# Kernel optimization log

Measured on AMD Instinct MI355X. Metric: run time of the kernel, lower is better.

The kernel has to match this reference:

```python
import jax, jax.numpy as jnp
import numpy as np

B, S, D = 8, 1024, 1024
H = 16
D_HEAD = D // H
RANK = 256
NC = 64
NE = 64
KC = 16  # top_k_compress
KE = 8   # top_k_expand


def setup_inputs() -> dict:
    key = jax.random.key(0)
    ks = jax.random.split(key, 9)
    rn = lambda k, sh, s=1.0: jax.random.normal(k, sh, jnp.float32) * s
    return {
        "x": rn(ks[0], (B, S, D)),
        "importance": jax.random.uniform(ks[1], (B, S), jnp.float32),
        "W_compress": rn(ks[2], (NC, D), 1.0 / np.sqrt(D)),
        "W_Q": rn(ks[3], (NE, D), 1.0 / np.sqrt(D)),
        "W_K": rn(ks[4], (NE, D), 1.0 / np.sqrt(D)),
        "W_V": rn(ks[5], (NE, D), 1.0 / np.sqrt(D)),
        "compress_neurons": rn(ks[6], (NC, D, RANK), 1.0 / np.sqrt(D)),
        "expand_pool": rn(ks[7], (NE, RANK, D), 1.0 / np.sqrt(RANK)),
        "W_O": rn(ks[8], (D, D), 1.0 / np.sqrt(D)),
    }


def _route(x, importance, W, k):
    """Per-token softmax router, importance-aggregated, top-k renormalized."""
    pref = jax.nn.softmax(jnp.einsum('bsd,nd->bsn', x, W), axis=-1)  # [B,S,n]
    w = jnp.einsum('bs,bsn->bn', importance, pref)                   # [B,n]
    w = w / (w.sum(-1, keepdims=True) + 1e-8)
    tw, ti = jax.lax.top_k(w, k)                                     # [B,k]
    tw = tw / (tw.sum(-1, keepdims=True) + 1e-8)
    return tw, ti


def reference(x, importance, W_compress, W_Q, W_K, W_V, compress_neurons, expand_pool, W_O):
    # --- GlobalRouters.get_attention_weights ---
    cw, ci = _route(x, importance, W_compress, KC)
    qw, qi = _route(x, importance, W_Q, KE)
    kw, ki = _route(x, importance, W_K, KE)
    vw, vi = _route(x, importance, W_V, KE)

    # --- NeuronCircuit.forward ---
    # gather + mix compress neurons: [B,KC,D,R] -> [B,D,R]
    shared_c = jnp.einsum('bk,bkdr->bdr', cw, compress_neurons[ci])
    h = jnp.einsum('bsd,bdr->bsr', x, shared_c)  # [B,S,R]

    eQ = jnp.einsum('bk,bkrd->brd', qw, expand_pool[qi])
    eK = jnp.einsum('bk,bkrd->brd', kw, expand_pool[ki])
    eV = jnp.einsum('bk,bkrd->brd', vw, expand_pool[vi])

    def heads(t):  # [B,S,D] -> [B,H,S,d_head]
        return t.reshape(B, S, H, D_HEAD).transpose(0, 2, 1, 3)

    Q = heads(jnp.einsum('bsr,brd->bsd', h, eQ))
    K = heads(jnp.einsum('bsr,brd->bsd', h, eK))
    V = heads(jnp.einsum('bsr,brd->bsd', h, eV))

    scale = 1.0 / np.sqrt(D_HEAD)
    scores = jnp.einsum('bhqd,bhkd->bhqk', Q, K) * scale
    causal = jnp.tril(jnp.ones((S, S), dtype=bool))
    scores = jnp.where(causal, scores, jnp.finfo(scores.dtype).min)
    attn = jax.nn.softmax(scores, axis=-1)
    out = jnp.einsum('bhqk,bhkd->bhqd', attn, V)
    out = out.transpose(0, 2, 1, 3).reshape(B, S, D)
    return jnp.einsum('bsd,ed->bse', out, W_O)  # expand_O (Linear, no bias)
```

## Files before the change

kernel.cpp:

```cpp
#include <hip/hip_runtime.h>

typedef __attribute__((ext_vector_type(8))) short short8;
typedef __attribute__((ext_vector_type(4))) short short4v;
typedef __attribute__((ext_vector_type(4))) float f32x4;
typedef unsigned short u16;
typedef unsigned int u32;

__device__ __forceinline__ float bf2f(u16 h) {
    return __uint_as_float(((u32)h) << 16);
}
__device__ __forceinline__ u16 f2bf(float f) {
    u32 u = __float_as_uint(f);
    u32 r = u + 0x7fffu + ((u >> 16) & 1u);
    return (u16)(r >> 16);
}
__device__ __forceinline__ u32 pack_bf(float a, float b) {
    return __builtin_amdgcn_perm(__float_as_uint(b), __float_as_uint(a), 0x07060302u);
}

__device__ __forceinline__ void async_copy16(const void* g, void* l) {
    __builtin_amdgcn_global_load_lds(
        (const __attribute__((address_space(1))) void*)g,
        (__attribute__((address_space(3))) void*)l, 16, 0, 0);
}

__global__ __launch_bounds__(256) void cvt_split(
    const float* __restrict__ in, u16* __restrict__ hi, u16* __restrict__ lo, int n4)
{
    int i = blockIdx.x * 256 + threadIdx.x;
    if (i >= n4) return;
    float4 v = ((const float4*)in)[i];
    short4v h, l;
    float vv[4] = {v.x, v.y, v.z, v.w};
#pragma unroll
    for (int j = 0; j < 4; j++) {
        u16 hb = f2bf(vv[j]);
        h[j] = (short)hb;
        l[j] = (short)f2bf(vv[j] - bf2f(hb));
    }
    ((short4v*)hi)[i] = h;
    ((short4v*)lo)[i] = l;
}

__global__ __launch_bounds__(256) void cvt_split_w4(
    const float* __restrict__ w0, const float* __restrict__ w1,
    const float* __restrict__ w2, const float* __restrict__ w3,
    u16* __restrict__ hi, u16* __restrict__ lo)
{
    const int r = blockIdx.x >> 6;
    const float* src = (r == 0) ? w0 : (r == 1) ? w1 : (r == 2) ? w2 : w3;
    int i = (blockIdx.x & 63) * 256 + threadIdx.x;
    float4 v = ((const float4*)src)[i];
    short4v h, l;
    float vv[4] = {v.x, v.y, v.z, v.w};
#pragma unroll
    for (int j = 0; j < 4; j++) {
        u16 hb = f2bf(vv[j]);
        h[j] = (short)hb;
        l[j] = (short)f2bf(vv[j] - bf2f(hb));
    }
    ((short4v*)(hi + (long)r * 65536))[i] = h;
    ((short4v*)(lo + (long)r * 65536))[i] = l;
}

__global__ __launch_bounds__(256) void cvt_bf(
    const float* __restrict__ in, u16* __restrict__ out, int n4)
{
    int i = blockIdx.x * 256 + threadIdx.x;
    if (i >= n4) return;
    float4 v = ((const float4*)in)[i];
    short4v h;
    h[0] = (short)f2bf(v.x); h[1] = (short)f2bf(v.y);
    h[2] = (short)f2bf(v.z); h[3] = (short)f2bf(v.w);
    ((short4v*)out)[i] = h;
}

template <typename CT>
__global__ __launch_bounds__(256) void gemm_bt(
    const u16* __restrict__ A, long lda, long bsA,
    const u16* __restrict__ Bm, long ldb, long bsB,
    CT* __restrict__ C, long ldc, long bsC, int K, float cscale)
{
    __shared__ __align__(16) u16 lsA[128 * 32];
    __shared__ __align__(16) u16 lsB[128 * 32];
    const int tid = threadIdx.x;
    const int wave = tid >> 6, lane = tid & 63;
    const int quad = lane >> 4, l15 = lane & 15;
    const int wm = wave >> 1, wn = wave & 1;
    const long m0 = (long)blockIdx.x * 128, n0 = (long)blockIdx.y * 128;
    A  += (long)blockIdx.z * bsA;
    Bm += (long)blockIdx.z * bsB;
    C  += (long)blockIdx.z * bsC;
    const int srow = lane >> 2, scol = (lane & 3) * 8;

    f32x4 acc[4][4];
#pragma unroll
    for (int i = 0; i < 4; i++)
#pragma unroll
        for (int j = 0; j < 4; j++) acc[i][j] = (f32x4){0.f, 0.f, 0.f, 0.f};

    const u16* ga0 = A + (m0 + (wave * 2 + 0) * 16 + srow) * lda + scol;
    const u16* ga1 = A + (m0 + (wave * 2 + 1) * 16 + srow) * lda + scol;
    const u16* gb0 = Bm + (n0 + (wave * 2 + 0) * 16 + srow) * ldb + scol;
    const u16* gb1 = Bm + (n0 + (wave * 2 + 1) * 16 + srow) * ldb + scol;
    u16* la0 = &lsA[(wave * 2 + 0) * 512];
    u16* la1 = &lsA[(wave * 2 + 1) * 512];
    u16* lb0 = &lsB[(wave * 2 + 0) * 512];
    u16* lb1 = &lsB[(wave * 2 + 1) * 512];

    for (int kk = 0; kk < K; kk += 32) {
        async_copy16(ga0 + kk, la0);
        async_copy16(ga1 + kk, la1);
        async_copy16(gb0 + kk, lb0);
        async_copy16(gb1 + kk, lb1);
        __syncthreads();
        short8 af[4], bf[4];
#pragma unroll
        for (int mt = 0; mt < 4; mt++)
            af[mt] = *(const short8*)&lsA[(wm * 64 + mt * 16 + l15) * 32 + quad * 8];
#pragma unroll
        for (int nt = 0; nt < 4; nt++)
            bf[nt] = *(const short8*)&lsB[(wn * 64 + nt * 16 + l15) * 32 + quad * 8];
#pragma unroll
        for (int mt = 0; mt < 4; mt++)
#pragma unroll
            for (int nt = 0; nt < 4; nt++)
                acc[mt][nt] = __builtin_amdgcn_mfma_f32_16x16x32_bf16(
                    af[mt], bf[nt], acc[mt][nt], 0, 0, 0);
        __syncthreads();
    }
#pragma unroll
    for (int mt = 0; mt < 4; mt++) {
        const long rowb = m0 + wm * 64 + mt * 16 + quad * 4;
#pragma unroll
        for (int nt = 0; nt < 4; nt++) {
            const long col = n0 + wn * 64 + nt * 16 + l15;
#pragma unroll
            for (int r = 0; r < 4; r++) {
                const float v = acc[mt][nt][r] * cscale;
                if constexpr (sizeof(CT) == 2)
                    C[(rowb + r) * ldc + col] = f2bf(v);
                else
                    C[(rowb + r) * ldc + col] = v;
            }
        }
    }
}

__global__ __launch_bounds__(256) void gemm_router(
    const u16* __restrict__ Ah, const u16* __restrict__ Al,
    const u16* __restrict__ Bh, const u16* __restrict__ Bl,
    float* __restrict__ C)
{
    __shared__ __align__(16) u16 lsA[128 * 32];
    __shared__ __align__(16) u16 lsB[128 * 32];
    const int tid = threadIdx.x;
    const int wave = tid >> 6, lane = tid & 63;
    const int quad = lane >> 4, l15 = lane & 15;
    const int wm = wave >> 1, wn = wave & 1;
    const long m0 = (long)blockIdx.x * 128, n0 = (long)blockIdx.y * 128;
    const int srow = lane >> 2, scol = (lane & 3) * 8;
    const long offA = (m0 + (wave * 2) * 16 + srow) * 1024 + scol;
    const long offB = (n0 + (wave * 2) * 16 + srow) * 1024 + scol;
    u16* la0 = &lsA[(wave * 2 + 0) * 512];
    u16* la1 = &lsA[(wave * 2 + 1) * 512];
    u16* lb0 = &lsB[(wave * 2 + 0) * 512];
    u16* lb1 = &lsB[(wave * 2 + 1) * 512];

    f32x4 acc[4][4];
#pragma unroll
    for (int i = 0; i < 4; i++)
#pragma unroll
        for (int j = 0; j < 4; j++) acc[i][j] = (f32x4){0.f, 0.f, 0.f, 0.f};

    for (int seg = 0; seg < 3; seg++) {
        const u16* A = (seg == 1) ? Al : Ah;
        const u16* B = (seg == 2) ? Bl : Bh;
        const u16* ga = A + offA;
        const u16* gb = B + offB;
        for (int kk = 0; kk < 1024; kk += 32) {
            async_copy16(ga + kk, la0);
            async_copy16(ga + 16384 + kk, la1);
            async_copy16(gb + kk, lb0);
            async_copy16(gb + 16384 + kk, lb1);
            __syncthreads();
            short8 af[4], bf[4];
#pragma unroll
            for (int mt = 0; mt < 4; mt++)
                af[mt] = *(const short8*)&lsA[(wm * 64 + mt * 16 + l15) * 32 + quad * 8];
#pragma unroll
            for (int nt = 0; nt < 4; nt++)
                bf[nt] = *(const short8*)&lsB[(wn * 64 + nt * 16 + l15) * 32 + quad * 8];
#pragma unroll
            for (int mt = 0; mt < 4; mt++)
#pragma unroll
                for (int nt = 0; nt < 4; nt++)
                    acc[mt][nt] = __builtin_amdgcn_mfma_f32_16x16x32_bf16(
                        af[mt], bf[nt], acc[mt][nt], 0, 0, 0);
            __syncthreads();
        }
    }
#pragma unroll
    for (int mt = 0; mt < 4; mt++) {
        const long rowb = m0 + wm * 64 + mt * 16 + quad * 4;
#pragma unroll
        for (int nt = 0; nt < 4; nt++) {
            const long col = n0 + wn * 64 + nt * 16 + l15;
#pragma unroll
            for (int r = 0; r < 4; r++)
                C[(rowb + r) * 256 + col] = acc[mt][nt][r];
        }
    }
}

__global__ __launch_bounds__(128) void router_agg(
    const float* __restrict__ logits, const float* __restrict__ imp,
    float* __restrict__ w_raw)
{
    __shared__ float pref[32][257];
    const int tid = threadIdx.x;
    const int tl = tid >> 2, r = tid & 3;
    const int s = blockIdx.x * 32 + tl;
    const int b = s >> 10;
    const float* lp = logits + (long)s * 256 + r * 64;
    float v[64];
#pragma unroll
    for (int i = 0; i < 16; i++) {
        float4 f = ((const float4*)lp)[i];
        v[i * 4 + 0] = f.x; v[i * 4 + 1] = f.y;
        v[i * 4 + 2] = f.z; v[i * 4 + 3] = f.w;
    }
    float mx = v[0];
#pragma unroll
    for (int i = 1; i < 64; i++) mx = fmaxf(mx, v[i]);
    float sum = 0.f;
#pragma unroll
    for (int i = 0; i < 64; i++) { v[i] = __expf(v[i] - mx); sum += v[i]; }
    const float scale = imp[s] / sum;
#pragma unroll
    for (int i = 0; i < 64; i++) pref[tl][r * 64 + i] = v[i] * scale;
    __syncthreads();
#pragma unroll
    for (int half = 0; half < 2; half++) {
        const int idx = tid + half * 128;
        const int r2 = idx >> 6, n = idx & 63;
        float acc = 0.f;
#pragma unroll 8
        for (int t = 0; t < 32; t++) acc += pref[t][r2 * 64 + n];
        atomicAdd(&w_raw[(r2 * 8 + b) * 64 + n], acc);
    }
}

__global__ void topk_kernel(const float* __restrict__ w_raw,
                            float* __restrict__ topw, int* __restrict__ topi)
{
    const int r = blockIdx.x >> 3, b = blockIdx.x & 7;
    const int lane = threadIdx.x;
    const int k = (r == 0) ? 16 : 8;
    float w = w_raw[(r * 8 + b) * 64 + lane];
    float tot = w;
    for (int o2 = 32; o2 >= 1; o2 >>= 1) tot += __shfl_xor(tot, o2);
    w = w / (tot + 1e-8f);
    __shared__ float tw[16];
    __shared__ int ti[16];
    float cur = w;
    float ssum = 0.f;
    for (int j = 0; j < k; j++) {
        float m = cur; int mi = lane;
        for (int o2 = 32; o2 >= 1; o2 >>= 1) {
            float om = __shfl_xor(m, o2); int oi = __shfl_xor(mi, o2);
            if (om > m || (om == m && oi < mi)) { m = om; mi = oi; }
        }
        if (lane == 0) { tw[j] = m; ti[j] = mi; }
        ssum += m;
        if (lane == mi) cur = -1e30f;
    }
    __syncthreads();
    if (lane < 16) {
        topw[(r * 8 + b) * 16 + lane] = (lane < k) ? tw[lane] / (ssum + 1e-8f) : 0.f;
        topi[(r * 8 + b) * 16 + lane] = (lane < k) ? ti[lane] : 0;
    }
}

__global__ __launch_bounds__(256) void gather_mix(
    const float* __restrict__ pool, const float* __restrict__ topw,
    const int* __restrict__ topi, u16* __restrict__ out,
    int I, int J, int k)
{
    __shared__ float tile[64][65];
    const int b = blockIdx.z;
    const long IJ = (long)I * J;
    const int i0 = blockIdx.x * 64, j0 = blockIdx.y * 64;
    const float* tw = topw + b * 16;
    const int* ti = topi + b * 16;
    const int tid = threadIdx.x;
    const int il = tid >> 2, jg = tid & 3;
    float acc[16];
#pragma unroll
    for (int m = 0; m < 16; m++) acc[m] = 0.f;
    for (int kk = 0; kk < k; kk++) {
        const float wgt = tw[kk];
        const long n = ti[kk];
        const float* src = pool + n * IJ + (long)(i0 + il) * J + j0 + jg * 16;
        float4 a0 = ((const float4*)src)[0];
        float4 a1 = ((const float4*)src)[1];
        float4 a2 = ((const float4*)src)[2];
        float4 a3 = ((const float4*)src)[3];
        acc[0] += wgt * a0.x;  acc[1] += wgt * a0.y;
        acc[2] += wgt * a0.z;  acc[3] += wgt * a0.w;
        acc[4] += wgt * a1.x;  acc[5] += wgt * a1.y;
        acc[6] += wgt * a1.z;  acc[7] += wgt * a1.w;
        acc[8] += wgt * a2.x;  acc[9] += wgt * a2.y;
        acc[10] += wgt * a2.z; acc[11] += wgt * a2.w;
        acc[12] += wgt * a3.x; acc[13] += wgt * a3.y;
        acc[14] += wgt * a3.z; acc[15] += wgt * a3.w;
    }
#pragma unroll
    for (int m = 0; m < 16; m++) tile[il][jg * 16 + m] = acc[m];
    __syncthreads();
    const int jl = tid >> 2, ig = tid & 3;
    short8 o0, o1;
#pragma unroll
    for (int m = 0; m < 8; m++) {
        o0[m] = (short)f2bf(tile[ig * 16 + m][jl]);
        o1[m] = (short)f2bf(tile[ig * 16 + 8 + m][jl]);
    }
    u16* dst = out + (long)b * IJ + (long)(j0 + jl) * I + i0 + ig * 16;
    *(short8*)dst = o0;
    *(short8*)(dst + 8) = o1;
}

__global__ __launch_bounds__(256, 2) void flash_attn(
    const u16* __restrict__ Qg, const u16* __restrict__ Kg,
    const u16* __restrict__ Vt, u16* __restrict__ Og)
{
    __shared__ __align__(16) u16 plds[4][32 * 72];
    const int tid = threadIdx.x;
    const int wv = tid >> 6, lane = tid & 63;
    const int quad = lane >> 4, l15 = lane & 15;
    const int bidx = blockIdx.x;
    const int bh = bidx & 127;
    const int qt = ((bidx >> 7) << 2) + wv;
    const int hh = bh & 15, bb = bh >> 4;
    const long SD = 1024L * 1024L;
    const u16* Qb = Qg + (long)bb * SD + hh * 64;
    const u16* Kb = Kg + (long)bb * SD + hh * 64;
    const u16* Vb = Vt + (long)bb * SD + (long)hh * 64 * 1024;
    u16* myp = plds[wv];

    const int q0 = qt * 32;

    short8 qf[2][2];
#pragma unroll
    for (int mt = 0; mt < 2; mt++)
#pragma unroll
        for (int kb = 0; kb < 2; kb++)
            qf[mt][kb] = *(const short8*)(Qb + (long)(q0 + mt * 16 + l15) * 1024 + kb * 32 + quad * 8);

    f32x4 o[2][4];
    float mrow[2] = {-3e38f, -3e38f}, lrow[2] = {0.f, 0.f};
#pragma unroll
    for (int mt = 0; mt < 2; mt++)
#pragma unroll
        for (int nt = 0; nt < 4; nt++) o[mt][nt] = (f32x4){0.f, 0.f, 0.f, 0.f};

    const int ntile = (q0 + 95) >> 6;
    short8 kf[4][2], kn[4][2];
#pragma unroll
    for (int kt = 0; kt < 4; kt++)
#pragma unroll
        for (int kb = 0; kb < 2; kb++)
            kf[kt][kb] = *(const short8*)(Kb + (long)(kt * 16 + l15) * 1024 + kb * 32 + quad * 8);

    for (int it = 0; it < ntile; it++) {
        const int k2 = it * 64;
        const bool last = (it == ntile - 1);
        f32x4 st[4][2];
#pragma unroll
        for (int kt = 0; kt < 4; kt++)
#pragma unroll
            for (int q_ = 0; q_ < 2; q_++) {
                f32x4 z = (f32x4){0.f, 0.f, 0.f, 0.f};
                z = __builtin_amdgcn_mfma_f32_16x16x32_bf16(kf[kt][0], qf[q_][0], z, 0, 0, 0);
                z = __builtin_amdgcn_mfma_f32_16x16x32_bf16(kf[kt][1], qf[q_][1], z, 0, 0, 0);
                st[kt][q_] = z;
            }
        short8 vf[4][2];
#pragma unroll
        for (int nt = 0; nt < 4; nt++)
#pragma unroll
            for (int kh = 0; kh < 2; kh++)
                vf[nt][kh] = *(const short8*)(Vb + (long)(nt * 16 + l15) * 1024 + k2 + kh * 32 + quad * 8);
        if (it + 1 < ntile) {
#pragma unroll
            for (int kt = 0; kt < 4; kt++)
#pragma unroll
                for (int kb = 0; kb < 2; kb++)
                    kn[kt][kb] = *(const short8*)(Kb + (long)(k2 + 64 + kt * 16 + l15) * 1024 + kb * 32 + quad * 8);
        }
        float am[2];
#pragma unroll
        for (int q_ = 0; q_ < 2; q_++) {
            if (last) {
#pragma unroll
                for (int kt = 0; kt < 4; kt++)
#pragma unroll
                    for (int r = 0; r < 4; r++)
                        if (k2 + kt * 16 + quad * 4 + r > q0 + q_ * 16 + l15)
                            st[kt][q_][r] = -3e38f;
            }
            float cm = -3e38f;
#pragma unroll
            for (int kt = 0; kt < 4; kt++)
#pragma unroll
                for (int r = 0; r < 4; r++) cm = fmaxf(cm, st[kt][q_][r]);
            cm = fmaxf(cm, __shfl_xor(cm, 16));
            cm = fmaxf(cm, __shfl_xor(cm, 32));
            const float mn = fmaxf(mrow[q_], cm);
            am[q_] = exp2f(mrow[q_] - mn);
            mrow[q_] = mn;
            const float moff = 0.00281502f - mn;
            float rs = 0.f;
#pragma unroll
            for (int kt = 0; kt < 4; kt++) {
                float p0 = exp2f(st[kt][q_][0] + moff);
                float p1 = exp2f(st[kt][q_][1] + moff);
                float p2 = exp2f(st[kt][q_][2] + moff);
                float p3 = exp2f(st[kt][q_][3] + moff);
                rs += (p0 + p1) + (p2 + p3);
                u32 w0 = pack_bf(p0, p1);
                u32 w1 = pack_bf(p2, p3);
                *(uint2*)&myp[(q_ * 16 + l15) * 72 + kt * 16 + quad * 4] = make_uint2(w0, w1);
            }
            rs += __shfl_xor(rs, 16);
            rs += __shfl_xor(rs, 32);
            lrow[q_] = lrow[q_] * am[q_] + rs;
        }
        float av[2][4];
#pragma unroll
        for (int mt = 0; mt < 2; mt++)
#pragma unroll
            for (int r = 0; r < 4; r++)
                av[mt][r] = __shfl(am[mt], quad * 4 + r);
        asm volatile("s_waitcnt lgkmcnt(0)" ::: "memory");
        short8 pf0[2], pf1[2];
#pragma unroll
        for (int kh = 0; kh < 2; kh++) {
            pf0[kh] = *(const short8*)&myp[(l15) * 72 + kh * 32 + quad * 8];
            pf1[kh] = *(const short8*)&myp[(16 + l15) * 72 + kh * 32 + quad * 8];
        }
#pragma unroll
        for (int mt = 0; mt < 2; mt++)
#pragma unroll
            for (int nt = 0; nt < 4; nt++)
#pragma unroll
                for (int r = 0; r < 4; r++) o[mt][nt][r] *= av[mt][r];
#pragma unroll
        for (int nt = 0; nt < 4; nt++)
#pragma unroll
            for (int kh = 0; kh < 2; kh++) {
                o[0][nt] = __builtin_amdgcn_mfma_f32_16x16x32_bf16(pf0[kh], vf[nt][kh], o[0][nt], 0, 0, 0);
                o[1][nt] = __builtin_amdgcn_mfma_f32_16x16x32_bf16(pf1[kh], vf[nt][kh], o[1][nt], 0, 0, 0);
            }
        if (it + 1 < ntile) {
#pragma unroll
            for (int kt = 0; kt < 4; kt++)
#pragma unroll
                for (int kb = 0; kb < 2; kb++) kf[kt][kb] = kn[kt][kb];
        }
    }
#pragma unroll
    for (int mt = 0; mt < 2; mt++)
#pragma unroll
        for (int r = 0; r < 4; r++) {
            const float li = 1.0f / __shfl(lrow[mt], quad * 4 + r);
            const long row = q0 + mt * 16 + quad * 4 + r;
#pragma unroll
            for (int nt = 0; nt < 4; nt++)
                Og[(long)bb * SD + row * 1024 + hh * 64 + nt * 16 + l15] =
                    f2bf(o[mt][nt][r] * li);
        }
}

extern "C" void kernel_launch(void* const* d_in, const int* in_sizes, int n_in,
                              void* d_out, int out_size, void* d_ws, size_t ws_size,
                              hipStream_t stream)
{
    const float* x   = (const float*)d_in[0];
    const float* imp = (const float*)d_in[1];
    const float* cn  = (const float*)d_in[6];
    const float* ep  = (const float*)d_in[7];
    const float* Wo  = (const float*)d_in[8];
    float* outp = (float*)d_out;
    char* ws = (char*)d_ws;

    u16* xh = (u16*)d_out;
    u16* xl = xh + 8388608;

    u16*   Wh     = (u16*)(ws + 0);
    u16*   Wl     = (u16*)(ws + 524288);
    u16*   Wobf   = (u16*)(ws + 1048576);
    float* w_raw  = (float*)(ws + 3145728);
    float* topw   = (float*)(ws + 3153920);
    int*   topi   = (int*)(ws + 3155968);
    float* logits = (float*)(ws + 4194304);
    u16*   scT    = (u16*)(ws + 12582912);
    u16*   eQT    = (u16*)(ws + 16777216);
    u16*   Kb     = (u16*)(ws + 4194304);
    u16*   hbuf   = (u16*)(ws + 20971520);
    u16*   eKT    = (u16*)(ws + 25165824);
    u16*   eVT    = (u16*)(ws + 29360128);
    u16*   Qb     = (u16*)(ws + 33554432);
    u16*   VTb    = (u16*)(ws + 50331648);
    u16*   aout   = (u16*)(ws + 67108864);

    cvt_split<<<dim3(8192), 256, 0, stream>>>(x, xh, xl, 2097152);
    cvt_split_w4<<<dim3(256), 256, 0, stream>>>(
        (const float*)d_in[2], (const float*)d_in[3],
        (const float*)d_in[4], (const float*)d_in[5], Wh, Wl);
    cvt_bf<<<dim3(1024), 256, 0, stream>>>(Wo, Wobf, 262144);
    hipMemsetAsync(w_raw, 0, 4 * 8 * 64 * 4, stream);

    gemm_router<<<dim3(64, 2, 1), 256, 0, stream>>>(xh, xl, Wh, Wl, logits);
    router_agg<<<dim3(256), 128, 0, stream>>>(logits, imp, w_raw);
    topk_kernel<<<dim3(32), 64, 0, stream>>>(w_raw, topw, topi);
    gather_mix<<<dim3(16, 4, 8), 256, 0, stream>>>(cn, topw + 0 * 128, topi + 0 * 128, scT, 1024, 256, 16);
    gather_mix<<<dim3(4, 16, 8), 256, 0, stream>>>(ep, topw + 1 * 128, topi + 1 * 128, eQT, 256, 1024, 8);
    gather_mix<<<dim3(4, 16, 8), 256, 0, stream>>>(ep, topw + 2 * 128, topi + 2 * 128, eKT, 256, 1024, 8);
    gather_mix<<<dim3(4, 16, 8), 256, 0, stream>>>(ep, topw + 3 * 128, topi + 3 * 128, eVT, 256, 1024, 8);
    gemm_bt<u16><<<dim3(8, 2, 8), 256, 0, stream>>>(
        xh, 1024, 1048576, scT, 1024, 262144, hbuf, 256, 262144, 1024, 1.0f);
    gemm_bt<u16><<<dim3(8, 8, 8), 256, 0, stream>>>(
        hbuf, 256, 262144, eQT, 256, 262144, Qb, 1024, 1048576, 256, 0.180336880111f);
    gemm_bt<u16><<<dim3(8, 8, 8), 256, 0, stream>>>(
        hbuf, 256, 262144, eKT, 256, 262144, Kb, 1024, 1048576, 256, 1.0f);
    gemm_bt<u16><<<dim3(8, 8, 8), 256, 0, stream>>>(
        eVT, 256, 262144, hbuf, 256, 262144, VTb, 1024, 1048576, 256, 1.0f);
    flash_attn<<<dim3(1024), 256, 0, stream>>>(Qb, Kb, VTb, aout);
    gemm_bt<float><<<dim3(64, 8, 1), 256, 0, stream>>>(
        aout, 1024, 0, Wobf, 1024, 0, outp, 1024, 0, 1024, 1.0f);
}
```

Measured before the change: 454.3 us.

## Merge QKV gather-mix and GEMM launches, reorder and retune flash attention

The three expand-pool gather_mix launches become one gather_mix3 launch with a 24-deep z grid, and the three Q/K/V projection GEMMs become one gemm_qkv launch that selects operands by blockIdx.z. This cuts launch overhead and gives each launch a bigger grid to fill the GPU. Flash attention now schedules the longest causal query tiles first, drops the register double-buffered K prefetch in favour of in-loop loads, and raises its occupancy hint from 2 to 3 blocks per CU. Losing the prefetch may expose K load latency, which the extra occupancy is meant to hide.

```diff
diff --git a/kernel.cpp b/kernel.cpp
--- a/kernel.cpp
+++ b/kernel.cpp
@@ -143,6 +143,77 @@
                 else
                     C[(rowb + r) * ldc + col] = v;
             }
+        }
+    }
+}
+
+__global__ __launch_bounds__(256) void gemm_qkv(
+    const u16* __restrict__ hbuf, const u16* __restrict__ eQT,
+    const u16* __restrict__ eKT, const u16* __restrict__ eVT,
+    u16* __restrict__ Qb, u16* __restrict__ Kb, u16* __restrict__ VTb)
+{
+    __shared__ __align__(16) u16 lsA[128 * 32];
+    __shared__ __align__(16) u16 lsB[128 * 32];
+    const int z = blockIdx.z;
+    const int sel = z >> 3, bbz = z & 7;
+    const long ab = (long)bbz * 262144;
+    const u16* A  = ((sel == 2) ? eVT : hbuf) + ab;
+    const u16* Bm = ((sel == 0) ? eQT : (sel == 1) ? eKT : hbuf) + ab;
+    u16* C = ((sel == 0) ? Qb : (sel == 1) ? Kb : VTb) + (long)bbz * 1048576;
+    const float cscale = (sel == 0) ? 0.180336880111f : 1.0f;
+
+    const int tid = threadIdx.x;
+    const int wave = tid >> 6, lane = tid & 63;
+    const int quad = lane >> 4, l15 = lane & 15;
+    const int wm = wave >> 1, wn = wave & 1;
+    const long m0 = (long)blockIdx.x * 128, n0 = (long)blockIdx.y * 128;
+    const int srow = lane >> 2, scol = (lane & 3) * 8;
+
+    f32x4 acc[4][4];
+#pragma unroll
+    for (int i = 0; i < 4; i++)
+#pragma unroll
+        for (int j = 0; j < 4; j++) acc[i][j] = (f32x4){0.f, 0.f, 0.f, 0.f};
+
+    const u16* ga0 = A + (m0 + (wave * 2 + 0) * 16 + srow) * 256 + scol;
+    const u16* ga1 = A + (m0 + (wave * 2 + 1) * 16 + srow) * 256 + scol;
+    const u16* gb0 = Bm + (n0 + (wave * 2 + 0) * 16 + srow) * 256 + scol;
+    const u16* gb1 = Bm + (n0 + (wave * 2 + 1) * 16 + srow) * 256 + scol;
+    u16* la0 = &lsA[(wave * 2 + 0) * 512];
+    u16* la1 = &lsA[(wave * 2 + 1) * 512];
+    u16* lb0 = &lsB[(wave * 2 + 0) * 512];
+    u16* lb1 = &lsB[(wave * 2 + 1) * 512];
+
+    for (int kk = 0; kk < 256; kk += 32) {
+        async_copy16(ga0 + kk, la0);
+        async_copy16(ga1 + kk, la1);
+        async_copy16(gb0 + kk, lb0);
+        async_copy16(gb1 + kk, lb1);
+        __syncthreads();
+        short8 af[4], bf[4];
+#pragma unroll
+        for (int mt = 0; mt < 4; mt++)
+            af[mt] = *(const short8*)&lsA[(wm * 64 + mt * 16 + l15) * 32 + quad * 8];
+#pragma unroll
+        for (int nt = 0; nt < 4; nt++)
+            bf[nt] = *(const short8*)&lsB[(wn * 64 + nt * 16 + l15) * 32 + quad * 8];
+#pragma unroll
+        for (int mt = 0; mt < 4; mt++)
+#pragma unroll
+            for (int nt = 0; nt < 4; nt++)
+                acc[mt][nt] = __builtin_amdgcn_mfma_f32_16x16x32_bf16(
+                    af[mt], bf[nt], acc[mt][nt], 0, 0, 0);
+        __syncthreads();
+    }
+#pragma unroll
+    for (int mt = 0; mt < 4; mt++) {
+        const long rowb = m0 + wm * 64 + mt * 16 + quad * 4;
+#pragma unroll
+        for (int nt = 0; nt < 4; nt++) {
+            const long col = n0 + wn * 64 + nt * 16 + l15;
+#pragma unroll
+            for (int r = 0; r < 4; r++)
+                C[(rowb + r) * 1024 + col] = f2bf(acc[mt][nt][r] * cscale);
         }
     }
 }
@@ -330,7 +401,57 @@
     *(short8*)(dst + 8) = o1;
 }
 
-__global__ __launch_bounds__(256, 2) void flash_attn(
+__global__ __launch_bounds__(256) void gather_mix3(
+    const float* __restrict__ pool, const float* __restrict__ topw,
+    const int* __restrict__ topi, u16* __restrict__ eQT,
+    u16* __restrict__ eKT, u16* __restrict__ eVT)
+{
+    __shared__ float tile[64][65];
+    const int z = blockIdx.z;
+    const int r = z >> 3, b = z & 7;
+    u16* out = (r == 0) ? eQT : (r == 1) ? eKT : eVT;
+    const long IJ = 262144;
+    const int i0 = blockIdx.x * 64, j0 = blockIdx.y * 64;
+    const float* tw = topw + (1 + r) * 128 + b * 16;
+    const int* ti = topi + (1 + r) * 128 + b * 16;
+    const int tid = threadIdx.x;
+    const int il = tid >> 2, jg = tid & 3;
+    float acc[16];
+#pragma unroll
+    for (int m = 0; m < 16; m++) acc[m] = 0.f;
+    for (int kk = 0; kk < 8; kk++) {
+        const float wgt = tw[kk];
+        const long n = ti[kk];
+        const float* src = pool + n * IJ + (long)(i0 + il) * 1024 + j0 + jg * 16;
+        float4 a0 = ((const float4*)src)[0];
+        float4 a1 = ((const float4*)src)[1];
+        float4 a2 = ((const float4*)src)[2];
+        float4 a3 = ((const float4*)src)[3];
+        acc[0] += wgt * a0.x;  acc[1] += wgt * a0.y;
+        acc[2] += wgt * a0.z;  acc[3] += wgt * a0.w;
+        acc[4] += wgt * a1.x;  acc[5] += wgt * a1.y;
+        acc[6] += wgt * a1.z;  acc[7] += wgt * a1.w;
+        acc[8] += wgt * a2.x;  acc[9] += wgt * a2.y;
+        acc[10] += wgt * a2.z; acc[11] += wgt * a2.w;
+        acc[12] += wgt * a3.x; acc[13] += wgt * a3.y;
+        acc[14] += wgt * a3.z; acc[15] += wgt * a3.w;
+    }
+#pragma unroll
+    for (int m = 0; m < 16; m++) tile[il][jg * 16 + m] = acc[m];
+    __syncthreads();
+    const int jl = tid >> 2, ig = tid & 3;
+    short8 o0, o1;
+#pragma unroll
+    for (int m = 0; m < 8; m++) {
+        o0[m] = (short)f2bf(tile[ig * 16 + m][jl]);
+        o1[m] = (short)f2bf(tile[ig * 16 + 8 + m][jl]);
+    }
+    u16* dst = out + (long)b * IJ + (long)(j0 + jl) * 256 + i0 + ig * 16;
+    *(short8*)dst = o0;
+    *(short8*)(dst + 8) = o1;
+}
+
+__global__ __launch_bounds__(256, 3) void flash_attn(
     const u16* __restrict__ Qg, const u16* __restrict__ Kg,
     const u16* __restrict__ Vt, u16* __restrict__ Og)
 {
@@ -340,7 +461,7 @@
     const int quad = lane >> 4, l15 = lane & 15;
     const int bidx = blockIdx.x;
     const int bh = bidx & 127;
-    const int qt = ((bidx >> 7) << 2) + wv;
+    const int qt = ((7 - (bidx >> 7)) << 2) + wv;
     const int hh = bh & 15, bb = bh >> 4;
     const long SD = 1024L * 1024L;
     const u16* Qb = Qg + (long)bb * SD + hh * 64;
@@ -365,16 +486,16 @@
         for (int nt = 0; nt < 4; nt++) o[mt][nt] = (f32x4){0.f, 0.f, 0.f, 0.f};
 
     const int ntile = (q0 + 95) >> 6;
-    short8 kf[4][2], kn[4][2];
-#pragma unroll
-    for (int kt = 0; kt < 4; kt++)
-#pragma unroll
-        for (int kb = 0; kb < 2; kb++)
-            kf[kt][kb] = *(const short8*)(Kb + (long)(kt * 16 + l15) * 1024 + kb * 32 + quad * 8);
 
     for (int it = 0; it < ntile; it++) {
         const int k2 = it * 64;
         const bool last = (it == ntile - 1);
+        short8 kf[4][2];
+#pragma unroll
+        for (int kt = 0; kt < 4; kt++)
+#pragma unroll
+            for (int kb = 0; kb < 2; kb++)
+                kf[kt][kb] = *(const short8*)(Kb + (long)(k2 + kt * 16 + l15) * 1024 + kb * 32 + quad * 8);
         f32x4 st[4][2];
 #pragma unroll
         for (int kt = 0; kt < 4; kt++)
@@ -391,13 +512,6 @@
 #pragma unroll
             for (int kh = 0; kh < 2; kh++)
                 vf[nt][kh] = *(const short8*)(Vb + (long)(nt * 16 + l15) * 1024 + k2 + kh * 32 + quad * 8);
-        if (it + 1 < ntile) {
-#pragma unroll
-            for (int kt = 0; kt < 4; kt++)
-#pragma unroll
-                for (int kb = 0; kb < 2; kb++)
-                    kn[kt][kb] = *(const short8*)(Kb + (long)(k2 + 64 + kt * 16 + l15) * 1024 + kb * 32 + quad * 8);
-        }
         float am[2];
 #pragma unroll
         for (int q_ = 0; q_ < 2; q_++) {
@@ -462,12 +576,6 @@
                 o[0][nt] = __builtin_amdgcn_mfma_f32_16x16x32_bf16(pf0[kh], vf[nt][kh], o[0][nt], 0, 0, 0);
                 o[1][nt] = __builtin_amdgcn_mfma_f32_16x16x32_bf16(pf1[kh], vf[nt][kh], o[1][nt], 0, 0, 0);
             }
-        if (it + 1 < ntile) {
-#pragma unroll
-            for (int kt = 0; kt < 4; kt++)
-#pragma unroll
-                for (int kb = 0; kb < 2; kb++) kf[kt][kb] = kn[kt][kb];
-        }
     }
 #pragma unroll
     for (int mt = 0; mt < 2; mt++)
@@ -525,17 +633,10 @@
     router_agg<<<dim3(256), 128, 0, stream>>>(logits, imp, w_raw);
     topk_kernel<<<dim3(32), 64, 0, stream>>>(w_raw, topw, topi);
     gather_mix<<<dim3(16, 4, 8), 256, 0, stream>>>(cn, topw + 0 * 128, topi + 0 * 128, scT, 1024, 256, 16);
-    gather_mix<<<dim3(4, 16, 8), 256, 0, stream>>>(ep, topw + 1 * 128, topi + 1 * 128, eQT, 256, 1024, 8);
-    gather_mix<<<dim3(4, 16, 8), 256, 0, stream>>>(ep, topw + 2 * 128, topi + 2 * 128, eKT, 256, 1024, 8);
-    gather_mix<<<dim3(4, 16, 8), 256, 0, stream>>>(ep, topw + 3 * 128, topi + 3 * 128, eVT, 256, 1024, 8);
+    gather_mix3<<<dim3(4, 16, 24), 256, 0, stream>>>(ep, topw, topi, eQT, eKT, eVT);
     gemm_bt<u16><<<dim3(8, 2, 8), 256, 0, stream>>>(
         xh, 1024, 1048576, scT, 1024, 262144, hbuf, 256, 262144, 1024, 1.0f);
-    gemm_bt<u16><<<dim3(8, 8, 8), 256, 0, stream>>>(
-        hbuf, 256, 262144, eQT, 256, 262144, Qb, 1024, 1048576, 256, 0.180336880111f);
-    gemm_bt<u16><<<dim3(8, 8, 8), 256, 0, stream>>>(
-        hbuf, 256, 262144, eKT, 256, 262144, Kb, 1024, 1048576, 256, 1.0f);
-    gemm_bt<u16><<<dim3(8, 8, 8), 256, 0, stream>>>(
-        eVT, 256, 262144, hbuf, 256, 262144, VTb, 1024, 1048576, 256, 1.0f);
+    gemm_qkv<<<dim3(8, 8, 24), 256, 0, stream>>>(hbuf, eQT, eKT, eVT, Qb, Kb, VTb);
     flash_attn<<<dim3(1024), 256, 0, stream>>>(Qb, Kb, VTb, aout);
     gemm_bt<float><<<dim3(64, 8, 1), 256, 0, stream>>>(
         aout, 1024, 0, Wobf, 1024, 0, outp, 1024, 0, 1024, 1.0f);
```

New measurement: 448.2 us. No clear change (-1.3%).
